# Optimization experiments

Measured on AMD Instinct MI355X. Metric: run time of the kernel, lower is better.

The kernel has to match this reference:

```python
import jax, jax.numpy as jnp
import numpy as np

R3D = (0.1, 0.2, 0.4)
R6D = (0.15, 0.25, 0.45)
K = 64  # max_num_neighbors in radius()


def setup_inputs() -> dict:
    key = jax.random.key(0)
    k1, k2, k3, k4 = jax.random.split(key, 4)
    B, M = 8, 2048
    pos = jax.random.uniform(k1, (B, M, 3), dtype=jnp.float32)        # points in unit cube
    x = 0.05 * jax.random.normal(k2, (B, M, 3), dtype=jnp.float32)    # predicted coords/features
    w = 0.5 * jax.random.normal(k3, (1, len(R3D)), dtype=jnp.float32)  # lin1.weight [1, S]
    b = 0.1 * jax.random.normal(k4, (1,), dtype=jnp.float32)           # lin1.bias [1]
    return {"x": x, "pos": pos, "w": w, "b": b}


def _radius_knn(P, r, k=K):
    # P: [B, M, D]. Returns (idx, mask): k nearest neighbors per point (incl. self)
    # and a mask of those actually within radius r (== torch_cluster.radius with
    # max_num_neighbors=k, deterministic nearest-first selection).
    sq = jnp.sum(P * P, axis=-1)                                   # [B, M]
    d2 = sq[:, :, None] + sq[:, None, :] - 2.0 * jnp.einsum('bmd,bnd->bmn', P, P)
    neg_vals, idx = jax.lax.top_k(-d2, k)                          # k smallest distances
    mask = (-neg_vals) <= r * r                                    # [B, M, k]
    return idx, mask


def _gather(v, idx):
    # v: [B, M, D], idx: [B, M, k] -> [B, M, k, D]
    B = v.shape[0]
    return v[jnp.arange(B)[:, None, None], idx]


def reference(x, pos, w, b):
    B, M, _ = x.shape
    pos_ext = jnp.concatenate([pos, x], axis=-1)                   # [B, M, 6]
    msgs = []
    for r3, r6 in zip(R3D, R6D):
        # 6D radius graph -> scatter_mean of x over neighbors
        idx6, m6 = _radius_knn(pos_ext, r6)                        # [B, M, K]
        xs = _gather(x, idx6)                                      # [B, M, K, 3]
        cnt6 = jnp.sum(m6, axis=-1).astype(x.dtype)                # >=1 (self edge)
        x_centers = jnp.sum(xs * m6[..., None], axis=2) / cnt6[..., None]  # [B, M, 3]
        # 3D radius graph -> mean of ||x_centers_i - x_centers_j|| per node
        idx3, m3 = _radius_knn(pos, r3)                            # [B, M, K]
        diff = x_centers[:, :, None, :] - _gather(x_centers, idx3)  # [B, M, K, 3]
        s = jnp.sum(diff * diff, axis=-1)
        d = jnp.sqrt(jnp.maximum(s, 1e-12))                        # safe norm (grad at 0)
        cnt3 = jnp.sum(m3, axis=-1).astype(x.dtype)
        msgs.append(jnp.sum(d * m3, axis=-1) / cnt3)               # [B, M]
    msg = jnp.stack(msgs, axis=-1)                                 # [B, M, S]
    conf = jax.nn.sigmoid(jnp.einsum('bms,os->bmo', msg, w) + b)   # [B, M, 1]
    return conf[..., 0].reshape(B * M)                             # flat [N], like conf[:, 0]
```

## Files before the change

kernel.cpp:

```cpp
#include <hip/hip_runtime.h>
#include <math.h>

#define MPTS 2048
#define NBATCH 8
#define NT 32
#define KMAX 64
#define NBIN 128
#define BCAP 24
#define TPB 512

typedef unsigned short u16;
typedef unsigned int u32;
typedef unsigned long long u64;

static __device__ __forceinline__ int mbcnt64(u64 m) {
  return __builtin_amdgcn_mbcnt_hi((u32)(m >> 32),
                                   __builtin_amdgcn_mbcnt_lo((u32)m, 0));
}

template <bool COMPACT>
__global__ __launch_bounds__(TPB, 6) void kernelA(
    const float* __restrict__ x, const float* __restrict__ pos,
    float4* __restrict__ xci, float* __restrict__ tau3, u16* __restrict__ nbr) {
  __shared__ __align__(16) float4 P4[MPTS];
  __shared__ __align__(16) float2 X2[MPTS];
  __shared__ __align__(16) u32 histAll[8 * NBIN];

  const int tid  = threadIdx.x;
  const int wv   = tid >> 6;
  const int lane = tid & 63;
  const int pt   = wv >> 1;
  const int mtr  = wv & 1;
  const int wid  = blockIdx.x * 4 + pt;
  const int b    = wid >> 11;
  const int i    = wid & (MPTS - 1);
  const float* posb = pos + b * MPTS * 3;
  const float* xb   = x   + b * MPTS * 3;

  for (int p = tid; p < MPTS; p += TPB) {
    P4[p] = make_float4(posb[3*p+0], posb[3*p+1], posb[3*p+2], xb[3*p+0]);
    X2[p] = make_float2(xb[3*p+1], xb[3*p+2]);
  }
  ((uint2*)histAll)[tid] = make_uint2(0u, 0u);
  __syncthreads();

  u32* hw = &histAll[wv * NBIN];

  const float4 pi4 = P4[i];
  const float2 xi2 = X2[i];
  const float2 c0 = make_float2(pi4.x, pi4.y);
  const float2 c1 = make_float2(pi4.z, pi4.w);
  const float2 c2 = xi2;

  const float R2 = mtr ? 0.2025f : 0.16f;
  const float SC = mtr ? (128.0f / 0.2025f) : (128.0f / 0.16f);

  float da[NT];
  if (mtr == 0) {
#pragma unroll
    for (int k = 0; k < NT; ++k) {
      const int j = k * 64 + lane;
      const float4 pj = P4[j];
      const float2 d01 = make_float2(pj.x, pj.y) - c0;
      const float dz = pj.z - pi4.z;
      const float2 sq = d01 * d01;
      const float a = sq.x + sq.y + dz * dz;
      da[k] = a;
      const int bb = (int)(a * (128.0f / 0.16f));
      if ((u32)bb < 128u) atomicAdd(&hw[bb], 1u);
    }
  } else {
#pragma unroll
    for (int k = 0; k < NT; ++k) {
      const int j = k * 64 + lane;
      const float4 pj = P4[j];
      const float2 xj = X2[j];
      const float2 a0 = make_float2(pj.x, pj.y) - c0;
      const float2 a1 = make_float2(pj.z, pj.w) - c1;
      const float2 a2 = xj - c2;
      float2 s = a0 * a0;
      s += a1 * a1;
      s += a2 * a2;
      const float a = s.x + s.y;
      da[k] = a;
      const int bb = (int)(a * (128.0f / 0.2025f));
      if ((u32)bb < 128u) atomicAdd(&hw[bb], 1u);
    }
  }

  const u32 h0 = hw[2*lane], h1 = hw[2*lane+1];
  const u32 s2 = h0 + h1;
  u32 incl = s2;
#pragma unroll
  for (int off = 1; off < 64; off <<= 1) {
    const u32 tt = __shfl_up(incl, off, 64);
    if (lane >= off) incl += tt;
  }
  const u32 tot = __shfl(incl, 63, 64);
  float t = R2;

  if (tot > 64u) {
    const u32 excl = incl - s2;
    const u64 m = __ballot((excl < 64u) && (incl >= 64u));
    const int L = __builtin_ctzll(m);
    const u32 c0b = __shfl(excl, L, 64);
    const u32 g0 = __shfl(h0, L, 64);
    const u32 g1 = __shfl(h1, L, 64);
    int B; u32 cb, n;
    if (c0b + g0 >= 64u) { B = 2*L;     cb = c0b;      n = g0; }
    else                 { B = 2*L + 1; cb = c0b + g0; n = g1; }

    if (lane == 0) hw[0] = 0u;
    float* bv = (float*)&hw[1];

#pragma unroll
    for (int k = 0; k < NT; ++k) {
      const int bb = (int)(da[k] * SC);
      if (bb == B) {
        const u32 s = atomicAdd(&hw[0], 1u);
        if (s < (u32)BCAP) bv[s] = da[k];
      }
    }

    if (n <= (u32)BCAP) {
      const int nn = (int)n;
      const float v = (lane < nn) ? bv[lane] : 3.0e38f;
      u32 rank = 0;
      for (int cc = 0; cc < nn; ++cc) {
        const float w = __shfl(v, cc, 64);
        rank += ((w < v) || (w == v && cc < lane)) ? 1u : 0u;
      }
      const u64 sm = __ballot((lane < nn) && (rank == (u32)(63 - (int)cb)));
      t = __shfl(v, __builtin_ctzll(sm), 64);
    } else {
      float lo = (float)B * (R2 / (float)NBIN), hi = lo + R2 / (float)NBIN;
      for (int it = 0; it < 26; ++it) {
        const float mid = 0.5f * (lo + hi);
        int c = 0;
#pragma unroll
        for (int k = 0; k < NT; ++k) c += __popcll(__ballot(da[k] <= mid));
        if (c >= 64) { hi = mid; if (c == 64) break; } else lo = mid;
      }
      t = hi;
    }
  }

  u16* lw = (u16*)&hw[1 + BCAP];
  const float q0 = mtr ? 0.0225f : 0.01f;
  const float q1 = mtr ? 0.0625f : 0.04f;
  int base = 0;
#pragma unroll
  for (int k = 0; k < NT; ++k) {
    const int j = k * 64 + lane;
    const bool sel = (da[k] <= t);
    const u64 m = __ballot(sel);
    const int s = base + mbcnt64(m);
    if (sel && s < KMAX) {
      const int cl = (da[k] > q0) + (da[k] > q1);
      lw[s] = (u16)(j | (cl << 11));
    }
    base += __popcll(m);
  }
  const int cn = base < KMAX ? base : KMAX;

  if (mtr == 0) {
    if (COMPACT)
      nbr[(size_t)wid * KMAX + lane] = (lane < cn) ? lw[lane] : (u16)(3u << 11);
    if (lane == 0) tau3[wid] = t;
  } else {
    const u16 e = (lane < cn) ? lw[lane] : (u16)0xFFFF;
    const int cl = (e >> 11) & 3;
    const int jj = e & (MPTS - 1);
    const float xjx = P4[jj].w;
    const float2 xj = X2[jj];
    const bool v2 = (cl <= 2), v1 = (cl <= 1), v0 = (cl == 0);

    float2 v2a[6];
    v2a[0] = v0 ? make_float2(xjx, xj.x) : make_float2(0.f, 0.f);
    v2a[1] = v0 ? make_float2(xj.y, 1.f) : make_float2(0.f, 0.f);
    v2a[2] = v1 ? make_float2(xjx, xj.x) : make_float2(0.f, 0.f);
    v2a[3] = v1 ? make_float2(xj.y, 1.f) : make_float2(0.f, 0.f);
    v2a[4] = v2 ? make_float2(xjx, xj.x) : make_float2(0.f, 0.f);
    v2a[5] = v2 ? make_float2(xj.y, 1.f) : make_float2(0.f, 0.f);

#pragma unroll
    for (int v = 0; v < 6; ++v)
#pragma unroll
      for (int off = 32; off > 0; off >>= 1) {
        float2 o;
        o.x = __shfl_xor(v2a[v].x, off, 64);
        o.y = __shfl_xor(v2a[v].y, off, 64);
        v2a[v] += o;
      }

    if (lane == 0) {
#pragma unroll
      for (int s = 0; s < 3; ++s) {
        const float inv = 1.f / v2a[2*s+1].y;
        xci[(size_t)wid * 3 + s] =
            make_float4(v2a[2*s].x * inv, v2a[2*s].y * inv, v2a[2*s+1].x * inv, 0.f);
      }
    }
  }
}

__global__ __launch_bounds__(256) void kernelB_fast(
    const float4* __restrict__ xci, const float* __restrict__ wlin,
    const float* __restrict__ blin, const u16* __restrict__ nbr,
    float* __restrict__ out) {
  const int wid  = (blockIdx.x * 256 + threadIdx.x) >> 6;
  const int lane = threadIdx.x & 63;
  const int pbase = wid & ~(MPTS - 1);

  const u16 e = nbr[(size_t)wid * KMAX + lane];
  const int cl = e >> 11;
  const int gj = pbase + (e & (MPTS - 1));

  const float4 ci0 = xci[(size_t)wid*3 + 0];
  const float4 ci1 = xci[(size_t)wid*3 + 1];
  const float4 ci2 = xci[(size_t)wid*3 + 2];

  float s0 = 0.f, s1 = 0.f, s2 = 0.f, n0 = 0.f, n1 = 0.f, n2 = 0.f;
  if (cl <= 2) {
    const float4 cj2 = xci[(size_t)gj*3 + 2];
    float ux = ci2.x - cj2.x, uy = ci2.y - cj2.y, uz = ci2.z - cj2.z;
    s2 = sqrtf(fmaxf(ux*ux + uy*uy + uz*uz, 1e-12f)); n2 = 1.f;
    if (cl <= 1) {
      const float4 cj1 = xci[(size_t)gj*3 + 1];
      ux = ci1.x - cj1.x; uy = ci1.y - cj1.y; uz = ci1.z - cj1.z;
      s1 = sqrtf(fmaxf(ux*ux + uy*uy + uz*uz, 1e-12f)); n1 = 1.f;
      if (cl == 0) {
        const float4 cj0 = xci[(size_t)gj*3 + 0];
        ux = ci0.x - cj0.x; uy = ci0.y - cj0.y; uz = ci0.z - cj0.z;
        s0 = sqrtf(fmaxf(ux*ux + uy*uy + uz*uz, 1e-12f)); n0 = 1.f;
      }
    }
  }

  float vals[6] = {s0, s1, s2, n0, n1, n2};
#pragma unroll
  for (int v = 0; v < 6; ++v)
#pragma unroll
    for (int off = 32; off > 0; off >>= 1)
      vals[v] += __shfl_xor(vals[v], off, 64);

  if (lane == 0) {
    const float msg0 = vals[0] / vals[3];
    const float msg1 = vals[1] / vals[4];
    const float msg2 = vals[2] / vals[5];
    const float z = wlin[0]*msg0 + wlin[1]*msg1 + wlin[2]*msg2 + blin[0];
    out[wid] = 1.f / (1.f + expf(-z));
  }
}

__global__ __launch_bounds__(256) void kernelB_slow(
    const float* __restrict__ pos, const float* __restrict__ wlin,
    const float* __restrict__ blin, const float4* __restrict__ xci,
    const float* __restrict__ tau3, float* __restrict__ out) {
  const int wid  = (blockIdx.x * 256 + threadIdx.x) >> 6;
  const int lane = threadIdx.x & 63;
  const int b = wid >> 11;
  const int i = wid & (MPTS - 1);
  const float* posb = pos + b * MPTS * 3;
  const int pbase = b * MPTS;

  const float pix = posb[3*i+0], piy = posb[3*i+1], piz = posb[3*i+2];
  const float t3 = tau3[wid];
  const float thr0 = fminf(0.01f, t3);
  const float thr1 = fminf(0.04f, t3);

  const float4 ci0 = xci[(size_t)wid*3 + 0];
  const float4 ci1 = xci[(size_t)wid*3 + 1];
  const float4 ci2 = xci[(size_t)wid*3 + 2];

  float s0=0.f, s1=0.f, s2=0.f, n0=0.f, n1=0.f, n2=0.f;
  for (int k = 0; k < NT; ++k) {
    const int j = k * 64 + lane;
    const float dx = posb[3*j+0] - pix;
    const float dy = posb[3*j+1] - piy;
    const float dz = posb[3*j+2] - piz;
    const float a3 = dx*dx + dy*dy + dz*dz;
    if (a3 <= t3) {
      const float4 cj2 = xci[(size_t)(pbase + j)*3 + 2];
      float ux = ci2.x-cj2.x, uy = ci2.y-cj2.y, uz = ci2.z-cj2.z;
      s2 += sqrtf(fmaxf(ux*ux+uy*uy+uz*uz, 1e-12f)); n2 += 1.f;
      if (a3 <= thr1) {
        const float4 cj1 = xci[(size_t)(pbase + j)*3 + 1];
        ux = ci1.x-cj1.x; uy = ci1.y-cj1.y; uz = ci1.z-cj1.z;
        s1 += sqrtf(fmaxf(ux*ux+uy*uy+uz*uz, 1e-12f)); n1 += 1.f;
        if (a3 <= thr0) {
          const float4 cj0 = xci[(size_t)(pbase + j)*3 + 0];
          ux = ci0.x-cj0.x; uy = ci0.y-cj0.y; uz = ci0.z-cj0.z;
          s0 += sqrtf(fmaxf(ux*ux+uy*uy+uz*uz, 1e-12f)); n0 += 1.f;
        }
      }
    }
  }

  float vals[6] = {s0, s1, s2, n0, n1, n2};
#pragma unroll
  for (int v = 0; v < 6; ++v)
#pragma unroll
    for (int off = 32; off > 0; off >>= 1)
      vals[v] += __shfl_xor(vals[v], off, 64);

  if (lane == 0) {
    const float msg0 = vals[0] / vals[3];
    const float msg1 = vals[1] / vals[4];
    const float msg2 = vals[2] / vals[5];
    const float z = wlin[0]*msg0 + wlin[1]*msg1 + wlin[2]*msg2 + blin[0];
    out[wid] = 1.f / (1.f + expf(-z));
  }
}

extern "C" void kernel_launch(void* const* d_in, const int* in_sizes, int n_in,
                              void* d_out, int out_size, void* d_ws, size_t ws_size,
                              hipStream_t stream) {
  (void)in_sizes; (void)n_in; (void)out_size;
  const float* x    = (const float*)d_in[0];
  const float* pos  = (const float*)d_in[1];
  const float* wlin = (const float*)d_in[2];
  const float* blin = (const float*)d_in[3];
  float* out = (float*)d_out;

  const size_t npts = (size_t)NBATCH * MPTS;
  const size_t xci_bytes = npts * 3 * sizeof(float4);
  const size_t tau_bytes = npts * sizeof(float);
  const size_t nbr_bytes = npts * KMAX * sizeof(u16);
  float4* xci = (float4*)d_ws;
  float* tau3 = (float*)((char*)d_ws + xci_bytes);
  u16* nbr    = (u16*)((char*)d_ws + xci_bytes + tau_bytes);
  const bool fast = ws_size >= xci_bytes + tau_bytes + nbr_bytes;

  const int nblocksA = (int)(npts / 4);
  const int nblocksB = (int)(npts * 64 / 256);
  if (fast) {
    kernelA<true><<<nblocksA, TPB, 0, stream>>>(x, pos, xci, tau3, nbr);
    kernelB_fast<<<nblocksB, 256, 0, stream>>>(xci, wlin, blin, nbr, out);
  } else {
    kernelA<false><<<nblocksA, TPB, 0, stream>>>(x, pos, xci, tau3, nbr);
    kernelB_slow<<<nblocksB, 256, 0, stream>>>(pos, wlin, blin, xci, tau3, out);
  }
}
```

Before: 83.71 us.

## Split each point's neighbor search across two wavefronts with shared histograms

kernelA now uses 1024-thread blocks, and each (point, metric) task is split across two wavefronts. Each wavefront handles half the candidate points, so it keeps 16 distances in registers instead of 32. The wavefronts share an LDS histogram, a bin buffer and atomic list counters, with block-wide barriers between the phases. The bisection fallback used when the threshold bin overflows the buffer is replaced by taking the bin's upper edge, with the buffer capacity raised to make that rarer. This trades lower register pressure and more parallelism for extra barriers, atomics, non-deterministic neighbor order, and an approximate threshold in the overflow case.

```diff
diff --git a/kernel.cpp b/kernel.cpp
--- a/kernel.cpp
+++ b/kernel.cpp
@@ -3,11 +3,11 @@
 
 #define MPTS 2048
 #define NBATCH 8
-#define NT 32
+#define NT 16
 #define KMAX 64
 #define NBIN 128
-#define BCAP 24
-#define TPB 512
+#define BCAP 32
+#define TPB 1024
 
 typedef unsigned short u16;
 typedef unsigned int u32;
@@ -19,18 +19,23 @@
 }
 
 template <bool COMPACT>
-__global__ __launch_bounds__(TPB, 6) void kernelA(
+__global__ __launch_bounds__(TPB, 8) void kernelA(
     const float* __restrict__ x, const float* __restrict__ pos,
     float4* __restrict__ xci, float* __restrict__ tau3, u16* __restrict__ nbr) {
   __shared__ __align__(16) float4 P4[MPTS];
   __shared__ __align__(16) float2 X2[MPTS];
-  __shared__ __align__(16) u32 histAll[8 * NBIN];
+  __shared__ __align__(16) u32 hist[4][2][NBIN];
+  __shared__ float bv[4][2][BCAP];
+  __shared__ u32 bcnt[4][2];
+  __shared__ u32 lcnt[4][2];
+  __shared__ u16 lst6[4][KMAX];
 
   const int tid  = threadIdx.x;
   const int wv   = tid >> 6;
   const int lane = tid & 63;
-  const int pt   = wv >> 1;
-  const int mtr  = wv & 1;
+  const int pt   = wv >> 2;
+  const int mtr  = (wv >> 1) & 1;
+  const int half = wv & 1;
   const int wid  = blockIdx.x * 4 + pt;
   const int b    = wid >> 11;
   const int i    = wid & (MPTS - 1);
@@ -41,10 +46,11 @@
     P4[p] = make_float4(posb[3*p+0], posb[3*p+1], posb[3*p+2], xb[3*p+0]);
     X2[p] = make_float2(xb[3*p+1], xb[3*p+2]);
   }
-  ((uint2*)histAll)[tid] = make_uint2(0u, 0u);
+  ((u32*)hist)[tid]   = 0u;
+  if (tid < 16) { ((u32*)bcnt)[tid] = 0u; ((u32*)lcnt)[tid] = 0u; }
   __syncthreads();
 
-  u32* hw = &histAll[wv * NBIN];
+  u32* hw = hist[pt][mtr];
 
   const float4 pi4 = P4[i];
   const float2 xi2 = X2[i];
@@ -54,12 +60,13 @@
 
   const float R2 = mtr ? 0.2025f : 0.16f;
   const float SC = mtr ? (128.0f / 0.2025f) : (128.0f / 0.16f);
+  const int j0 = half * 64 + lane;
 
   float da[NT];
   if (mtr == 0) {
 #pragma unroll
     for (int k = 0; k < NT; ++k) {
-      const int j = k * 64 + lane;
+      const int j = k * 128 + j0;
       const float4 pj = P4[j];
       const float2 d01 = make_float2(pj.x, pj.y) - c0;
       const float dz = pj.z - pi4.z;
@@ -72,7 +79,7 @@
   } else {
 #pragma unroll
     for (int k = 0; k < NT; ++k) {
-      const int j = k * 64 + lane;
+      const int j = k * 128 + j0;
       const float4 pj = P4[j];
       const float2 xj = X2[j];
       const float2 a0 = make_float2(pj.x, pj.y) - c0;
@@ -87,6 +94,7 @@
       if ((u32)bb < 128u) atomicAdd(&hw[bb], 1u);
     }
   }
+  __syncthreads();
 
   const u32 h0 = hw[2*lane], h1 = hw[2*lane+1];
   const u32 s2 = h0 + h1;
@@ -98,6 +106,7 @@
   }
   const u32 tot = __shfl(incl, 63, 64);
   float t = R2;
+  int B = -1; u32 cb = 0, n = 0;
 
   if (tot > 64u) {
     const u32 excl = incl - s2;
@@ -106,25 +115,24 @@
     const u32 c0b = __shfl(excl, L, 64);
     const u32 g0 = __shfl(h0, L, 64);
     const u32 g1 = __shfl(h1, L, 64);
-    int B; u32 cb, n;
     if (c0b + g0 >= 64u) { B = 2*L;     cb = c0b;      n = g0; }
     else                 { B = 2*L + 1; cb = c0b + g0; n = g1; }
-
-    if (lane == 0) hw[0] = 0u;
-    float* bv = (float*)&hw[1];
 
 #pragma unroll
     for (int k = 0; k < NT; ++k) {
       const int bb = (int)(da[k] * SC);
       if (bb == B) {
-        const u32 s = atomicAdd(&hw[0], 1u);
-        if (s < (u32)BCAP) bv[s] = da[k];
-      }
-    }
-
+        const u32 s = atomicAdd(&bcnt[pt][mtr], 1u);
+        if (s < (u32)BCAP) bv[pt][mtr][s] = da[k];
+      }
+    }
+  }
+  __syncthreads();
+
+  if (tot > 64u) {
     if (n <= (u32)BCAP) {
       const int nn = (int)n;
-      const float v = (lane < nn) ? bv[lane] : 3.0e38f;
+      const float v = (lane < nn) ? bv[pt][mtr][lane] : 3.0e38f;
       u32 rank = 0;
       for (int cc = 0; cc < nn; ++cc) {
         const float w = __shfl(v, cc, 64);
@@ -133,42 +141,42 @@
       const u64 sm = __ballot((lane < nn) && (rank == (u32)(63 - (int)cb)));
       t = __shfl(v, __builtin_ctzll(sm), 64);
     } else {
-      float lo = (float)B * (R2 / (float)NBIN), hi = lo + R2 / (float)NBIN;
-      for (int it = 0; it < 26; ++it) {
-        const float mid = 0.5f * (lo + hi);
-        int c = 0;
-#pragma unroll
-        for (int k = 0; k < NT; ++k) c += __popcll(__ballot(da[k] <= mid));
-        if (c >= 64) { hi = mid; if (c == 64) break; } else lo = mid;
-      }
-      t = hi;
-    }
-  }
-
-  u16* lw = (u16*)&hw[1 + BCAP];
+      t = (float)(B + 1) * (R2 / (float)NBIN);
+    }
+  }
+
   const float q0 = mtr ? 0.0225f : 0.01f;
   const float q1 = mtr ? 0.0625f : 0.04f;
-  int base = 0;
 #pragma unroll
   for (int k = 0; k < NT; ++k) {
-    const int j = k * 64 + lane;
+    const int j = k * 128 + j0;
     const bool sel = (da[k] <= t);
     const u64 m = __ballot(sel);
-    const int s = base + mbcnt64(m);
+    const int c = __popcll(m);
+    u32 wbase = 0;
+    if (lane == 0 && c) wbase = atomicAdd(&lcnt[pt][mtr], (u32)c);
+    wbase = __shfl(wbase, 0, 64);
+    const int s = (int)wbase + mbcnt64(m);
     if (sel && s < KMAX) {
       const int cl = (da[k] > q0) + (da[k] > q1);
-      lw[s] = (u16)(j | (cl << 11));
-    }
-    base += __popcll(m);
-  }
-  const int cn = base < KMAX ? base : KMAX;
-
-  if (mtr == 0) {
-    if (COMPACT)
-      nbr[(size_t)wid * KMAX + lane] = (lane < cn) ? lw[lane] : (u16)(3u << 11);
+      const u16 e = (u16)(j | (cl << 11));
+      if (mtr == 0) {
+        if (COMPACT) nbr[(size_t)wid * KMAX + s] = e;
+      } else {
+        lst6[pt][s] = e;
+      }
+    }
+  }
+  __syncthreads();
+
+  if (mtr == 0 && half == 0) {
+    const int cn = (int)lcnt[pt][0] < KMAX ? (int)lcnt[pt][0] : KMAX;
+    if (COMPACT && lane >= cn)
+      nbr[(size_t)wid * KMAX + lane] = (u16)(3u << 11);
     if (lane == 0) tau3[wid] = t;
-  } else {
-    const u16 e = (lane < cn) ? lw[lane] : (u16)0xFFFF;
+  } else if (mtr == 1 && half == 0) {
+    const int cn = (int)lcnt[pt][1] < KMAX ? (int)lcnt[pt][1] : KMAX;
+    const u16 e = (lane < cn) ? lst6[pt][lane] : (u16)0xFFFF;
     const int cl = (e >> 11) & 3;
     const int jj = e & (MPTS - 1);
     const float xjx = P4[jj].w;
@@ -274,7 +282,7 @@
   const float4 ci2 = xci[(size_t)wid*3 + 2];
 
   float s0=0.f, s1=0.f, s2=0.f, n0=0.f, n1=0.f, n2=0.f;
-  for (int k = 0; k < NT; ++k) {
+  for (int k = 0; k < 32; ++k) {
     const int j = k * 64 + lane;
     const float dx = posb[3*j+0] - pix;
     const float dy = posb[3*j+1] - piy;
```

New measurement: 116.1 us. +38.7%, slower.
